# Performance work log

Measured on AMD Instinct MI355X. Metric: run time of the kernel, lower is better.

The kernel has to match this reference:

```python
import jax, jax.numpy as jnp
import numpy as np

LN_EPS = 1e-5  # torch LayerNorm default
EPSILON = 1e-8  # slot attention epsilon


def layer_norm(x, g, b):
    mu = jnp.mean(x, axis=-1, keepdims=True)
    var = jnp.var(x, axis=-1, keepdims=True)
    return (x - mu) * jax.lax.rsqrt(var + LN_EPS) * g + b


def setup_inputs() -> dict:
    key = jax.random.key(0)
    ks = jax.random.split(key, 12)
    B, N, S, D, M = 64, 4096, 8, 256, 1024
    s = 0.02
    return {
        "features": jax.random.normal(ks[0], (B, N, D), jnp.float32),
        "slots_init": jax.random.normal(ks[1], (B, S, D), jnp.float32),
        # LayerNorm params (feature, slots, mlp)
        "g_feat": jnp.ones((D,), jnp.float32), "b_feat": jnp.zeros((D,), jnp.float32),
        "g_slots": jnp.ones((D,), jnp.float32), "b_slots": jnp.zeros((D,), jnp.float32),
        "g_mlp": jnp.ones((D,), jnp.float32), "b_mlp": jnp.zeros((D,), jnp.float32),
        # k/v/q projections (torch Linear weight: [out,in], no bias)
        "Wk": jax.random.normal(ks[2], (D, D), jnp.float32) * s,
        "Wv": jax.random.normal(ks[3], (D, D), jnp.float32) * s,
        "Wq": jax.random.normal(ks[4], (D, D), jnp.float32) * s,
        # GRUCell params: weight_ih/hh [3D, D] (gate order r, z, n), biases [3D]
        "w_ih": jax.random.normal(ks[5], (3 * D, D), jnp.float32) * s,
        "w_hh": jax.random.normal(ks[6], (3 * D, D), jnp.float32) * s,
        "b_ih": jnp.zeros((3 * D,), jnp.float32),
        "b_hh": jnp.zeros((3 * D,), jnp.float32),
        # MLP: Linear(D->M), ReLU, Linear(M->D)
        "W1": jax.random.normal(ks[7], (M, D), jnp.float32) * s,
        "b1": jnp.zeros((M,), jnp.float32),
        "W2": jax.random.normal(ks[8], (D, M), jnp.float32) * s,
        "b2": jnp.zeros((D,), jnp.float32),
        "num_iter": 3,
    }


def gru_cell(x, h, w_ih, w_hh, b_ih, b_hh):
    # x, h: [B*, D]; torch.nn.GRUCell math, gate order r, z, n
    gi = x @ w_ih.T + b_ih  # [B*, 3D]
    gh = h @ w_hh.T + b_hh
    i_r, i_z, i_n = jnp.split(gi, 3, axis=-1)
    h_r, h_z, h_n = jnp.split(gh, 3, axis=-1)
    r = jax.nn.sigmoid(i_r + h_r)
    z = jax.nn.sigmoid(i_z + h_z)
    n = jnp.tanh(i_n + r * h_n)
    return (1.0 - z) * n + z * h


def reference(features, slots_init, g_feat, b_feat, g_slots, b_slots, g_mlp, b_mlp,
              Wk, Wv, Wq, w_ih, w_hh, b_ih, b_hh, W1, b1, W2, b2, num_iter):
    feats = layer_norm(features, g_feat, b_feat)          # [B, N, D]
    k = feats @ Wk.T                                      # [B, N, D]
    v = feats @ Wv.T                                      # [B, N, D]
    B, N, D = v.shape
    scale = D ** -0.5
    slots = slots_init                                    # [B, S, D]
    S = slots.shape[1]
    attn = None
    for _ in range(num_iter):
        slots_prev = slots
        q = layer_norm(slots, g_slots, b_slots) @ Wq.T    # [B, S, D]
        attn_logits = jnp.einsum('bid,bjd->bij', q, k) * scale  # [B, S, N]
        attn = jax.nn.softmax(attn_logits, axis=1)        # softmax over slots
        attn = attn + EPSILON
        attn_wm = attn / jnp.sum(attn, axis=-1, keepdims=True)
        updates = jnp.einsum('bij,bjd->bid', attn_wm, v)  # [B, S, D]
        slots = gru_cell(updates.reshape(-1, D), slots_prev.reshape(-1, D),
                         w_ih, w_hh, b_ih, b_hh).reshape(B, S, D)
        h = jax.nn.relu(layer_norm(slots, g_mlp, b_mlp) @ W1.T + b1)
        slots = slots + h @ W2.T + b2
    return slots, attn
```

## Files before the change

### kernel.cpp

```cpp
#include <hip/hip_runtime.h>
#include <stdint.h>

typedef unsigned short u16;
typedef unsigned int u32;
typedef __bf16 bf16_t;
typedef bf16_t bf16x8 __attribute__((ext_vector_type(8)));
typedef float f32x4 __attribute__((ext_vector_type(4)));

#define DEV static __device__ __forceinline__

DEV float bf2f(u16 a) {
  union { u32 u; float f; } c; c.u = ((u32)a) << 16; return c.f;
}
DEV u16 f2bf(float f) {
  union { float f; u32 u; } c; c.f = f;
  return (u16)((c.u + 0x7FFFu + ((c.u >> 16) & 1u)) >> 16);
}
DEV f32x4 mfma16(bf16x8 a, bf16x8 b, f32x4 c) {
  return __builtin_amdgcn_mfma_f32_16x16x32_bf16(a, b, c, 0, 0, 0);
}
DEV float wave_sum(float v) {
#pragma unroll
  for (int off = 32; off > 0; off >>= 1) v += __shfl_xor(v, off, 64);
  return v;
}
DEV float sum16(float v) {
  v += __shfl_xor(v, 1, 64);
  v += __shfl_xor(v, 2, 64);
  v += __shfl_xor(v, 4, 64);
  v += __shfl_xor(v, 8, 64);
  return v;
}

__global__ void __launch_bounds__(256) init_prep(
    const float* __restrict__ Wk, const float* __restrict__ Wv,
    const float* __restrict__ slots_init,
    const float* __restrict__ Wq, const float* __restrict__ w_ih,
    const float* __restrict__ w_hh, const float* __restrict__ W1,
    const float* __restrict__ W2,
    float* __restrict__ slots,
    u16* __restrict__ wqb, u16* __restrict__ wihb, u16* __restrict__ whhb,
    u16* __restrict__ w1b, u16* __restrict__ w2b,
    u16* __restrict__ wvb, u16* __restrict__ wktb) {
  const int blk = blockIdx.x;
  const int tid = threadIdx.x;
  if (blk < 128) {
    const int idx = blk * 1024 + tid * 4;
    *(float4*)(slots + idx) = *(const float4*)(slots_init + idx);
  } else if (blk < 1152) {
    const int i = (blk - 128) * 1024 + tid * 4;
    const float* src; u16* dst; int off;
    if (i < 65536)       { src = Wq;   dst = wqb;  off = i; }
    else if (i < 262144) { src = w_ih; dst = wihb; off = i - 65536; }
    else if (i < 458752) { src = w_hh; dst = whhb; off = i - 262144; }
    else if (i < 720896) { src = W1;   dst = w1b;  off = i - 458752; }
    else if (i < 983040) { src = W2;   dst = w2b;  off = i - 720896; }
    else                 { src = Wv;   dst = wvb;  off = i - 983040; }
    float4 v = *(const float4*)(src + off);
    *(ushort4*)(dst + off) = make_ushort4(f2bf(v.x), f2bf(v.y), f2bf(v.z), f2bf(v.w));
  } else {
    __shared__ u16 tl[64][66];
    const int tb = blk - 1152;
    const int r0 = (tb >> 2) * 64;
    const int c0 = (tb & 3) * 64;
    const int r = tid >> 2;
    const int cseg = (tid & 3) * 16;
#pragma unroll
    for (int q = 0; q < 4; q++) {
      float4 v = *(const float4*)(Wk + (size_t)(r0 + r) * 256 + c0 + cseg + q * 4);
      tl[r][cseg + q * 4 + 0] = f2bf(v.x);
      tl[r][cseg + q * 4 + 1] = f2bf(v.y);
      tl[r][cseg + q * 4 + 2] = f2bf(v.z);
      tl[r][cseg + q * 4 + 3] = f2bf(v.w);
    }
    __syncthreads();
    const int c = tid >> 2;
    const int rseg = (tid & 3) * 16;
    u16 out[16];
#pragma unroll
    for (int j = 0; j < 16; j++) out[j] = tl[rseg + j][c];
#pragma unroll
    for (int q = 0; q < 4; q++)
      *(ushort4*)(wktb + (size_t)(c0 + c) * 256 + r0 + rseg + q * 4) =
          make_ushort4(out[q * 4], out[q * 4 + 1], out[q * 4 + 2], out[q * 4 + 3]);
  }
}

__global__ void __launch_bounds__(256) ln_feat(
    const float* __restrict__ feat, const float* __restrict__ g,
    const float* __restrict__ bia,
    u16* __restrict__ fbuf, u16* __restrict__ fbuf_t) {
  __shared__ u16 T[64 * 264];
  const int tid = threadIdx.x;
  const int M0 = blockIdx.x * 64;
  const int b = M0 >> 12;
  const int nb = M0 & 4095;

#pragma unroll 2
  for (int i = 0; i < 8; i++) {
    const int gr = i * 256 + tid;
    const int m = gr >> 5;
    const int kc = gr & 31;
    const float* fp = feat + (size_t)(M0 + m) * 256 + kc * 8;
    float4 a0 = *(const float4*)fp;
    float4 a1 = *(const float4*)(fp + 4);
    float t1 = a0.x + a0.y + a0.z + a0.w + a1.x + a1.y + a1.z + a1.w;
    float t2 = a0.x * a0.x + a0.y * a0.y + a0.z * a0.z + a0.w * a0.w +
               a1.x * a1.x + a1.y * a1.y + a1.z * a1.z + a1.w * a1.w;
    t1 += __shfl_xor(t1, 1, 64);  t2 += __shfl_xor(t2, 1, 64);
    t1 += __shfl_xor(t1, 2, 64);  t2 += __shfl_xor(t2, 2, 64);
    t1 += __shfl_xor(t1, 4, 64);  t2 += __shfl_xor(t2, 4, 64);
    t1 += __shfl_xor(t1, 8, 64);  t2 += __shfl_xor(t2, 8, 64);
    t1 += __shfl_xor(t1, 16, 64); t2 += __shfl_xor(t2, 16, 64);
    const float mu = t1 * (1.f / 256.f);
    const float rs = rsqrtf(t2 * (1.f / 256.f) - mu * mu + 1e-5f);
    float4 g0 = *(const float4*)(g + kc * 8);
    float4 g1 = *(const float4*)(g + kc * 8 + 4);
    float4 b0 = *(const float4*)(bia + kc * 8);
    float4 b1 = *(const float4*)(bia + kc * 8 + 4);
    u16 y[8];
    y[0] = f2bf((a0.x - mu) * rs * g0.x + b0.x);
    y[1] = f2bf((a0.y - mu) * rs * g0.y + b0.y);
    y[2] = f2bf((a0.z - mu) * rs * g0.z + b0.z);
    y[3] = f2bf((a0.w - mu) * rs * g0.w + b0.w);
    y[4] = f2bf((a1.x - mu) * rs * g1.x + b1.x);
    y[5] = f2bf((a1.y - mu) * rs * g1.y + b1.y);
    y[6] = f2bf((a1.z - mu) * rs * g1.z + b1.z);
    y[7] = f2bf((a1.w - mu) * rs * g1.w + b1.w);
    uint4 pk = make_uint4((u32)y[0] | ((u32)y[1] << 16), (u32)y[2] | ((u32)y[3] << 16),
                          (u32)y[4] | ((u32)y[5] << 16), (u32)y[6] | ((u32)y[7] << 16));
    *(uint4*)&T[m * 264 + kc * 8] = pk;
    *(uint4*)(fbuf + (size_t)(M0 + m) * 256 + kc * 8) = pk;
  }
  __syncthreads();

  const int dl = tid >> 4;
  const int ns4 = (tid & 15) * 4;
#pragma unroll 4
  for (int o = 0; o < 16; o++) {
    const int d = dl + o * 16;
    u16 v0 = T[(ns4 + 0) * 264 + d];
    u16 v1 = T[(ns4 + 1) * 264 + d];
    u16 v2 = T[(ns4 + 2) * 264 + d];
    u16 v3 = T[(ns4 + 3) * 264 + d];
    *(ushort4*)(fbuf_t + ((size_t)b * 256 + d) * 4096 + nb + ns4) = make_ushort4(v0, v1, v2, v3);
  }
}

__global__ void __launch_bounds__(256) attn_pass(
    const float* __restrict__ slots, const float* __restrict__ gs, const float* __restrict__ bs,
    const u16* __restrict__ wqb, const u16* __restrict__ wktb,
    const u16* __restrict__ fbuf, const u16* __restrict__ fbuf_t,
    float* __restrict__ part_acc, float* __restrict__ part_den,
    float* __restrict__ attn_out, int store_attn) {
  __shared__ u16 pt[16 * 264];
  __shared__ u16 qld[16 * 264];
  const int chunk = blockIdx.x;
  const int b = blockIdx.y;
  const int n0 = chunk * 256;
  const int tid = threadIdx.x;
  const int lane = tid & 63;
  const int wv = tid >> 6;
  const int cl = lane & 15;
  const int rq = lane >> 4;
  const f32x4 Z = {0.f, 0.f, 0.f, 0.f};

  for (int i = tid; i < 8 * 264; i += 256) pt[8 * 264 + i] = 0;
  for (int rr = 0; rr < 2; rr++) {
    const int s = wv * 2 + rr;
    float4 x4 = *(const float4*)(slots + ((size_t)b * 8 + s) * 256 + lane * 4);
    float x[4] = {x4.x, x4.y, x4.z, x4.w};
    float s1 = x[0] + x[1] + x[2] + x[3];
    float s2 = x[0] * x[0] + x[1] * x[1] + x[2] * x[2] + x[3] * x[3];
    s1 = wave_sum(s1);
    s2 = wave_sum(s2);
    float mu = s1 * (1.f / 256.f);
    float rstd = rsqrtf(s2 * (1.f / 256.f) - mu * mu + 1e-5f);
    float4 g4 = *(const float4*)(gs + lane * 4);
    float4 b4 = *(const float4*)(bs + lane * 4);
    u16 o4[4];
    o4[0] = f2bf((x[0] - mu) * rstd * g4.x + b4.x);
    o4[1] = f2bf((x[1] - mu) * rstd * g4.y + b4.y);
    o4[2] = f2bf((x[2] - mu) * rstd * g4.z + b4.z);
    o4[3] = f2bf((x[3] - mu) * rstd * g4.w + b4.w);
    *(ushort4*)&pt[s * 264 + lane * 4] = make_ushort4(o4[0], o4[1], o4[2], o4[3]);
  }
  __syncthreads();

  {
    bf16x8 af[8];
#pragma unroll
    for (int ks = 0; ks < 8; ks++)
      af[ks] = *(const bf16x8*)&pt[cl * 264 + ks * 32 + rq * 8];
#pragma unroll
    for (int t = 0; t < 4; t++) {
      const int of = wv * 64 + t * 16;
      f32x4 acc = Z;
#pragma unroll
      for (int ks = 0; ks < 8; ks++) {
        bf16x8 bw = *(const bf16x8*)(wqb + (size_t)(of + cl) * 256 + ks * 32 + rq * 8);
        acc = mfma16(af[ks], bw, acc);
      }
#pragma unroll
      for (int r = 0; r < 4; r++)
        qld[(rq * 4 + r) * 264 + of + cl] = f2bf(acc[r]);
    }
  }
  __syncthreads();

  {
    bf16x8 a2[8];
#pragma unroll
    for (int ks = 0; ks < 8; ks++)
      a2[ks] = *(const bf16x8*)&qld[cl * 264 + ks * 32 + rq * 8];
#pragma unroll
    for (int t = 0; t < 4; t++) {
      const int of = wv * 64 + t * 16;
      f32x4 acc = Z;
#pragma unroll
      for (int ks = 0; ks < 8; ks++) {
        bf16x8 bw = *(const bf16x8*)(wktb + (size_t)(of + cl) * 256 + ks * 32 + rq * 8);
        acc = mfma16(a2[ks], bw, acc);
      }
#pragma unroll
      for (int r = 0; r < 4; r++)
        pt[(rq * 4 + r) * 264 + of + cl] = f2bf(acc[r]);
    }
  }
  __syncthreads();

  bf16x8 aq[8];
#pragma unroll
  for (int ks = 0; ks < 8; ks++)
    aq[ks] = *(const bf16x8*)&pt[cl * 264 + ks * 32 + rq * 8];

  float dacc[4] = {0.f, 0.f, 0.f, 0.f};
#pragma unroll
  for (int t = 0; t < 4; t++) {
    const int nl = (wv * 4 + t) * 16;
    f32x4 acc = Z;
    const int n = n0 + nl + cl;
#pragma unroll
    for (int ks = 0; ks < 8; ks++) {
      bf16x8 bk = *(const bf16x8*)(fbuf + ((size_t)b * 4096 + n) * 256 + ks * 32 + rq * 8);
      acc = mfma16(aq[ks], bk, acc);
    }
    float l[4];
#pragma unroll
    for (int r = 0; r < 4; r++) l[r] = acc[r] * 0.0625f;
    float m4 = fmaxf(fmaxf(l[0], l[1]), fmaxf(l[2], l[3]));
    float m8 = fmaxf(m4, __shfl_xor(m4, 16, 64));
    float e[4];
    float s4 = 0.f;
#pragma unroll
    for (int r = 0; r < 4; r++) { e[r] = __expf(l[r] - m8); s4 += e[r]; }
    float s8 = s4 + __shfl_xor(s4, 16, 64);
    float inv = 1.f / s8;
    float pa[4];
#pragma unroll
    for (int r = 0; r < 4; r++) pa[r] = e[r] * inv + 1e-8f;
#pragma unroll
    for (int r = 0; r < 4; r++) qld[(rq * 4 + r) * 264 + nl + cl] = f2bf(pa[r]);
    if (store_attn && lane < 32) {
#pragma unroll
      for (int r = 0; r < 4; r++)
        attn_out[((size_t)b * 8 + rq * 4 + r) * 4096 + n0 + nl + cl] = pa[r];
    }
#pragma unroll
    for (int r = 0; r < 4; r++) dacc[r] += sum16(pa[r]);
  }
  if (cl == 0 && lane < 32) {
#pragma unroll
    for (int r = 0; r < 4; r++)
      part_den[(((size_t)b * 16 + chunk) * 4 + wv) * 8 + rq * 4 + r] = dacc[r];
  }
  __syncthreads();

  bf16x8 ap[8];
#pragma unroll
  for (int ks = 0; ks < 8; ks++)
    ap[ks] = *(const bf16x8*)&qld[cl * 264 + ks * 32 + rq * 8];
#pragma unroll
  for (int t = 0; t < 4; t++) {
    const int df = wv * 64 + t * 16;
    f32x4 acc = Z;
    const int d = df + cl;
#pragma unroll
    for (int ks = 0; ks < 8; ks++) {
      bf16x8 bv = *(const bf16x8*)(fbuf_t + ((size_t)b * 256 + d) * 4096 + n0 + ks * 32 + rq * 8);
      acc = mfma16(ap[ks], bv, acc);
    }
    if (lane < 32) {
#pragma unroll
      for (int r = 0; r < 4; r++)
        part_acc[(((size_t)b * 16 + chunk) * 8 + rq * 4 + r) * 256 + d] = acc[r];
    }
  }
}

__global__ void __launch_bounds__(256) slot_update(
    const float* __restrict__ part_acc, const float* __restrict__ part_den,
    float* __restrict__ slots,
    const u16* __restrict__ wihb, const u16* __restrict__ whhb,
    const float* __restrict__ b_ih, const float* __restrict__ b_hh,
    const float* __restrict__ gm, const float* __restrict__ bm,
    const u16* __restrict__ w1b, const float* __restrict__ b1,
    const u16* __restrict__ w2b, const float* __restrict__ b2,
    const u16* __restrict__ wvb,
    float* __restrict__ slots_out, int last) {
  __shared__ u16 ubf[16 * 264];
  __shared__ u16 hbf[16 * 264];
  __shared__ u16 updbf[16 * 264];
  __shared__ float hf32[8 * 256];
  __shared__ float midf[8 * 256];
  __shared__ u16 h1bf[16 * 1032];
  __shared__ float denl[8];
  const int b = blockIdx.x;
  const int tid = threadIdx.x;
  const int lane = tid & 63;
  const int wv = tid >> 6;
  const int cl = lane & 15;
  const int rq = lane >> 4;
  const f32x4 Z = {0.f, 0.f, 0.f, 0.f};

  for (int i = tid; i < 8 * 264; i += 256) { ubf[8 * 264 + i] = 0; hbf[8 * 264 + i] = 0; }
  if (tid < 8) {
    float s = 0.f;
    for (int c = 0; c < 64; c++) s += part_den[((size_t)b * 64 + c) * 8 + tid];
    denl[tid] = s;
  }
  __syncthreads();

#pragma unroll
  for (int i = 0; i < 8; i++) {
    float s = 0.f;
#pragma unroll
    for (int c = 0; c < 16; c++)
      s += part_acc[(((size_t)b * 16 + c) * 8 + i) * 256 + tid];
    float u = s / denl[i];
    ubf[i * 264 + tid] = f2bf(u);
    float h = slots[((size_t)b * 8 + i) * 256 + tid];
    hf32[i * 256 + tid] = h;
    hbf[i * 264 + tid] = f2bf(h);
  }
  __syncthreads();

  {
    bf16x8 apf[8];
#pragma unroll
    for (int ks = 0; ks < 8; ks++)
      apf[ks] = *(const bf16x8*)&ubf[cl * 264 + ks * 32 + rq * 8];
#pragma unroll
    for (int t = 0; t < 4; t++) {
      const int of = wv * 64 + t * 16;
      f32x4 acc = Z;
#pragma unroll
      for (int ks = 0; ks < 8; ks++) {
        bf16x8 bw = *(const bf16x8*)(wvb + (size_t)(of + cl) * 256 + ks * 32 + rq * 8);
        acc = mfma16(apf[ks], bw, acc);
      }
#pragma unroll
      for (int r = 0; r < 4; r++)
        updbf[(rq * 4 + r) * 264 + of + cl] = f2bf(acc[r]);
    }
  }
  __syncthreads();

  bf16x8 au[8], ah[8];
#pragma unroll
  for (int ks = 0; ks < 8; ks++) {
    au[ks] = *(const bf16x8*)&updbf[cl * 264 + ks * 32 + rq * 8];
    ah[ks] = *(const bf16x8*)&hbf[cl * 264 + ks * 32 + rq * 8];
  }
#pragma unroll
  for (int j4 = 0; j4 < 4; j4++) {
    const int j = wv * 4 + j4;
    f32x4 a_ir = Z, a_iz = Z, a_in = Z, a_hr = Z, a_hz = Z, a_hn = Z;
#pragma unroll
    for (int ks = 0; ks < 8; ks++) {
      const int koff = ks * 32 + rq * 8;
      const int o_r = j * 16 + cl;
      bf16x8 bri = *(const bf16x8*)(wihb + (size_t)o_r * 256 + koff);
      bf16x8 bzi = *(const bf16x8*)(wihb + (size_t)(256 + o_r) * 256 + koff);
      bf16x8 bni = *(const bf16x8*)(wihb + (size_t)(512 + o_r) * 256 + koff);
      bf16x8 brh = *(const bf16x8*)(whhb + (size_t)o_r * 256 + koff);
      bf16x8 bzh = *(const bf16x8*)(whhb + (size_t)(256 + o_r) * 256 + koff);
      bf16x8 bnh = *(const bf16x8*)(whhb + (size_t)(512 + o_r) * 256 + koff);
      a_ir = mfma16(au[ks], bri, a_ir);
      a_iz = mfma16(au[ks], bzi, a_iz);
      a_in = mfma16(au[ks], bni, a_in);
      a_hr = mfma16(ah[ks], brh, a_hr);
      a_hz = mfma16(ah[ks], bzh, a_hz);
      a_hn = mfma16(ah[ks], bnh, a_hn);
    }
    if (lane < 32) {
      const int d = j * 16 + cl;
      const float bihr = b_ih[d], bihz = b_ih[256 + d], bihn = b_ih[512 + d];
      const float bhhr = b_hh[d], bhhz = b_hh[256 + d], bhhn = b_hh[512 + d];
#pragma unroll
      for (int r = 0; r < 4; r++) {
        const int s = rq * 4 + r;
        float ir = a_ir[r] + bihr, iz = a_iz[r] + bihz, inn = a_in[r] + bihn;
        float hr = a_hr[r] + bhhr, hz = a_hz[r] + bhhz, hn = a_hn[r] + bhhn;
        float rg = 1.f / (1.f + __expf(-(ir + hr)));
        float zg = 1.f / (1.f + __expf(-(iz + hz)));
        float ng = tanhf(inn + rg * hn);
        float h = hf32[s * 256 + d];
        midf[s * 256 + d] = (1.f - zg) * ng + zg * h;
      }
    }
  }
  __syncthreads();

  for (int rr = 0; rr < 2; rr++) {
    const int s = wv * 2 + rr;
    float4 x4 = *(const float4*)&midf[s * 256 + lane * 4];
    float x[4] = {x4.x, x4.y, x4.z, x4.w};
    float s1 = x[0] + x[1] + x[2] + x[3];
    float s2 = x[0] * x[0] + x[1] * x[1] + x[2] * x[2] + x[3] * x[3];
    s1 = wave_sum(s1);
    s2 = wave_sum(s2);
    float mu = s1 * (1.f / 256.f);
    float rstd = rsqrtf(s2 * (1.f / 256.f) - mu * mu + 1e-5f);
    float4 g4 = *(const float4*)(gm + lane * 4);
    float4 b4 = *(const float4*)(bm + lane * 4);
    u16 o4[4];
    o4[0] = f2bf((x[0] - mu) * rstd * g4.x + b4.x);
    o4[1] = f2bf((x[1] - mu) * rstd * g4.y + b4.y);
    o4[2] = f2bf((x[2] - mu) * rstd * g4.z + b4.z);
    o4[3] = f2bf((x[3] - mu) * rstd * g4.w + b4.w);
    *(ushort4*)&ubf[s * 264 + lane * 4] = make_ushort4(o4[0], o4[1], o4[2], o4[3]);
  }
  __syncthreads();

  bf16x8 al[8];
#pragma unroll
  for (int ks = 0; ks < 8; ks++)
    al[ks] = *(const bf16x8*)&ubf[cl * 264 + ks * 32 + rq * 8];
#pragma unroll
  for (int t = 0; t < 16; t++) {
    const int of = wv * 256 + t * 16;
    f32x4 acc = Z;
#pragma unroll
    for (int ks = 0; ks < 8; ks++) {
      bf16x8 bw = *(const bf16x8*)(w1b + (size_t)(of + cl) * 256 + ks * 32 + rq * 8);
      acc = mfma16(al[ks], bw, acc);
    }
    const float bb = b1[of + cl];
#pragma unroll
    for (int r = 0; r < 4; r++)
      h1bf[(rq * 4 + r) * 1032 + of + cl] = f2bf(fmaxf(acc[r] + bb, 0.f));
  }
  __syncthreads();

  f32x4 acc2[4] = {Z, Z, Z, Z};
  for (int ks = 0; ks < 32; ks++) {
    bf16x8 ah1 = *(const bf16x8*)&h1bf[cl * 1032 + ks * 32 + rq * 8];
#pragma unroll
    for (int t = 0; t < 4; t++) {
      const int o = wv * 64 + t * 16 + cl;
      bf16x8 bw = *(const bf16x8*)(w2b + (size_t)o * 1024 + ks * 32 + rq * 8);
      acc2[t] = mfma16(ah1, bw, acc2[t]);
    }
  }
  if (lane < 32) {
#pragma unroll
    for (int t = 0; t < 4; t++) {
      const int o = wv * 64 + t * 16 + cl;
      const float bb = b2[o];
#pragma unroll
      for (int r = 0; r < 4; r++) {
        const int s = rq * 4 + r;
        float val = midf[s * 256 + o] + acc2[t][r] + bb;
        slots[((size_t)b * 8 + s) * 256 + o] = val;
        if (last) slots_out[((size_t)b * 8 + s) * 256 + o] = val;
      }
    }
  }
}

extern "C" void kernel_launch(void* const* d_in, const int* in_sizes, int n_in,
                              void* d_out, int out_size, void* d_ws, size_t ws_size,
                              hipStream_t stream) {
  (void)in_sizes; (void)n_in; (void)out_size;
  const float* features = (const float*)d_in[0];
  const float* slots_init = (const float*)d_in[1];
  const float* g_feat = (const float*)d_in[2];
  const float* b_feat = (const float*)d_in[3];
  const float* g_slots = (const float*)d_in[4];
  const float* b_slots = (const float*)d_in[5];
  const float* g_mlp = (const float*)d_in[6];
  const float* b_mlp = (const float*)d_in[7];
  const float* Wk = (const float*)d_in[8];
  const float* Wv = (const float*)d_in[9];
  const float* Wq = (const float*)d_in[10];
  const float* w_ih = (const float*)d_in[11];
  const float* w_hh = (const float*)d_in[12];
  const float* b_ih = (const float*)d_in[13];
  const float* b_hh = (const float*)d_in[14];
  const float* W1 = (const float*)d_in[15];
  const float* b1 = (const float*)d_in[16];
  const float* W2 = (const float*)d_in[17];
  const float* b2 = (const float*)d_in[18];

  const size_t REQUIRED = 280236032ull;
  if (ws_size < REQUIRED) return;

  char* ws = (char*)d_ws;
  u16* fbuf = (u16*)(ws + 0);
  u16* fbuf_t = (u16*)(ws + 134217728);
  float* part_acc = (float*)(ws + 268959744);
  float* part_den = (float*)(ws + 277348352);
  float* slots = (float*)(ws + 277479424);
  u16* wktb = (u16*)(ws + 278003712);
  u16* wvb = (u16*)(ws + 278134784);
  u16* wqb = (u16*)(ws + 278269952);
  u16* wihb = (u16*)(ws + 278401024);
  u16* whhb = (u16*)(ws + 278794240);
  u16* w1b = (u16*)(ws + 279187456);
  u16* w2b = (u16*)(ws + 279711744);

  float* out_slots = (float*)d_out;
  float* out_attn = out_slots + 131072;

  init_prep<<<1168, 256, 0, stream>>>(Wk, Wv, slots_init, Wq, w_ih, w_hh, W1, W2,
                                      slots, wqb, wihb, whhb, w1b, w2b, wvb, wktb);
  ln_feat<<<4096, 256, 0, stream>>>(features, g_feat, b_feat, fbuf, fbuf_t);
  for (int it = 0; it < 3; it++) {
    attn_pass<<<dim3(16, 64), 256, 0, stream>>>(slots, g_slots, b_slots, wqb, wktb,
                                                fbuf, fbuf_t, part_acc, part_den,
                                                out_attn, it == 2 ? 1 : 0);
    slot_update<<<64, 256, 0, stream>>>(part_acc, part_den, slots, wihb, whhb, b_ih, b_hh,
                                        g_mlp, b_mlp, w1b, b1, w2b, b2, wvb,
                                        out_slots, it == 2 ? 1 : 0);
  }
}
```

Before: 891.4 us.

## Drop transposed feature buffer; stage feature tiles in swizzled LDS for both GEMMs

```diff
diff --git a/kernel.cpp b/kernel.cpp
--- a/kernel.cpp
+++ b/kernel.cpp
@@ -88,14 +88,9 @@
 
 __global__ void __launch_bounds__(256) ln_feat(
     const float* __restrict__ feat, const float* __restrict__ g,
-    const float* __restrict__ bia,
-    u16* __restrict__ fbuf, u16* __restrict__ fbuf_t) {
-  __shared__ u16 T[64 * 264];
+    const float* __restrict__ bia, u16* __restrict__ fbuf) {
   const int tid = threadIdx.x;
   const int M0 = blockIdx.x * 64;
-  const int b = M0 >> 12;
-  const int nb = M0 & 4095;
-
 #pragma unroll 2
   for (int i = 0; i < 8; i++) {
     const int gr = i * 256 + tid;
@@ -129,35 +124,17 @@
     y[7] = f2bf((a1.w - mu) * rs * g1.w + b1.w);
     uint4 pk = make_uint4((u32)y[0] | ((u32)y[1] << 16), (u32)y[2] | ((u32)y[3] << 16),
                           (u32)y[4] | ((u32)y[5] << 16), (u32)y[6] | ((u32)y[7] << 16));
-    *(uint4*)&T[m * 264 + kc * 8] = pk;
     *(uint4*)(fbuf + (size_t)(M0 + m) * 256 + kc * 8) = pk;
   }
-  __syncthreads();
-
-  const int dl = tid >> 4;
-  const int ns4 = (tid & 15) * 4;
-#pragma unroll 4
-  for (int o = 0; o < 16; o++) {
-    const int d = dl + o * 16;
-    u16 v0 = T[(ns4 + 0) * 264 + d];
-    u16 v1 = T[(ns4 + 1) * 264 + d];
-    u16 v2 = T[(ns4 + 2) * 264 + d];
-    u16 v3 = T[(ns4 + 3) * 264 + d];
-    *(ushort4*)(fbuf_t + ((size_t)b * 256 + d) * 4096 + nb + ns4) = make_ushort4(v0, v1, v2, v3);
-  }
-}
-
-__global__ void __launch_bounds__(256) attn_pass(
+}
+
+__global__ void __launch_bounds__(256) slot_qk(
     const float* __restrict__ slots, const float* __restrict__ gs, const float* __restrict__ bs,
     const u16* __restrict__ wqb, const u16* __restrict__ wktb,
-    const u16* __restrict__ fbuf, const u16* __restrict__ fbuf_t,
-    float* __restrict__ part_acc, float* __restrict__ part_den,
-    float* __restrict__ attn_out, int store_attn) {
-  __shared__ u16 pt[16 * 264];
+    u16* __restrict__ qkbuf) {
+  __shared__ u16 lnb[16 * 264];
   __shared__ u16 qld[16 * 264];
-  const int chunk = blockIdx.x;
-  const int b = blockIdx.y;
-  const int n0 = chunk * 256;
+  const int b = blockIdx.x;
   const int tid = threadIdx.x;
   const int lane = tid & 63;
   const int wv = tid >> 6;
@@ -165,7 +142,8 @@
   const int rq = lane >> 4;
   const f32x4 Z = {0.f, 0.f, 0.f, 0.f};
 
-  for (int i = tid; i < 8 * 264; i += 256) pt[8 * 264 + i] = 0;
+  for (int i = tid; i < 8 * 264; i += 256) lnb[8 * 264 + i] = 0;
+
   for (int rr = 0; rr < 2; rr++) {
     const int s = wv * 2 + rr;
     float4 x4 = *(const float4*)(slots + ((size_t)b * 8 + s) * 256 + lane * 4);
@@ -183,7 +161,7 @@
     o4[1] = f2bf((x[1] - mu) * rstd * g4.y + b4.y);
     o4[2] = f2bf((x[2] - mu) * rstd * g4.z + b4.z);
     o4[3] = f2bf((x[3] - mu) * rstd * g4.w + b4.w);
-    *(ushort4*)&pt[s * 264 + lane * 4] = make_ushort4(o4[0], o4[1], o4[2], o4[3]);
+    *(ushort4*)&lnb[s * 264 + lane * 4] = make_ushort4(o4[0], o4[1], o4[2], o4[3]);
   }
   __syncthreads();
 
@@ -191,7 +169,7 @@
     bf16x8 af[8];
 #pragma unroll
     for (int ks = 0; ks < 8; ks++)
-      af[ks] = *(const bf16x8*)&pt[cl * 264 + ks * 32 + rq * 8];
+      af[ks] = *(const bf16x8*)&lnb[cl * 264 + ks * 32 + rq * 8];
 #pragma unroll
     for (int t = 0; t < 4; t++) {
       const int of = wv * 64 + t * 16;
@@ -224,25 +202,53 @@
       }
 #pragma unroll
       for (int r = 0; r < 4; r++)
-        pt[(rq * 4 + r) * 264 + of + cl] = f2bf(acc[r]);
-    }
-  }
-  __syncthreads();
+        qkbuf[(size_t)b * 4096 + (rq * 4 + r) * 256 + of + cl] = f2bf(acc[r]);
+    }
+  }
+}
+
+__global__ void __launch_bounds__(256) attn_pass(
+    const u16* __restrict__ qkbuf, const u16* __restrict__ fbuf,
+    float* __restrict__ part_acc, float* __restrict__ part_den,
+    float* __restrict__ attn_out, int store_attn) {
+  __shared__ u16 Asm[64 * 264];
+  __shared__ u16 pt[16 * 72];
+  const int chunk = blockIdx.x;
+  const int b = blockIdx.y;
+  const int n0 = chunk * 64;
+  const int tid = threadIdx.x;
+  const int lane = tid & 63;
+  const int wv = tid >> 6;
+  const int cl = lane & 15;
+  const int rq = lane >> 4;
+  const f32x4 Z = {0.f, 0.f, 0.f, 0.f};
+
+  const u16* fsrc = fbuf + ((size_t)b * 4096 + n0) * 256;
+#pragma unroll
+  for (int i = 0; i < 8; i++) {
+    const int gr = i * 256 + tid;
+    const int m = gr >> 5;
+    const int kc = gr & 31;
+    uint4 v = *(const uint4*)(fsrc + (size_t)m * 256 + kc * 8);
+    const int sw = (kc & 24) | ((kc & 7) ^ (m & 7) ^ ((m >> 3) & 7));
+    *(uint4*)&Asm[m * 264 + sw * 8] = v;
+  }
 
   bf16x8 aq[8];
 #pragma unroll
   for (int ks = 0; ks < 8; ks++)
-    aq[ks] = *(const bf16x8*)&pt[cl * 264 + ks * 32 + rq * 8];
-
-  float dacc[4] = {0.f, 0.f, 0.f, 0.f};
-#pragma unroll
-  for (int t = 0; t < 4; t++) {
-    const int nl = (wv * 4 + t) * 16;
+    aq[ks] = *(const bf16x8*)(qkbuf + (size_t)b * 4096 + cl * 256 + ks * 32 + rq * 8);
+  __syncthreads();
+
+  {
+    const int nl = wv * 16;
+    const int n = nl + cl;
     f32x4 acc = Z;
-    const int n = n0 + nl + cl;
 #pragma unroll
     for (int ks = 0; ks < 8; ks++) {
-      bf16x8 bk = *(const bf16x8*)(fbuf + ((size_t)b * 4096 + n) * 256 + ks * 32 + rq * 8);
+      const int c = ks * 4 + rq;
+      const int ca = (c & 24) | ((c & 7) ^ (n & 7) ^ ((n >> 3) & 7));
+      bf16x8 bk = *(const bf16x8*)&Asm[n * 264 + ca * 8];
       acc = mfma16(aq[ks], bk, acc);
     }
     float l[4];
@@ -260,40 +266,46 @@
 #pragma unroll
     for (int r = 0; r < 4; r++) pa[r] = e[r] * inv + 1e-8f;
 #pragma unroll
-    for (int r = 0; r < 4; r++) qld[(rq * 4 + r) * 264 + nl + cl] = f2bf(pa[r]);
+    for (int r = 0; r < 4; r++) pt[(rq * 4 + r) * 72 + nl + cl] = f2bf(pa[r]);
     if (store_attn && lane < 32) {
 #pragma unroll
       for (int r = 0; r < 4; r++)
         attn_out[((size_t)b * 8 + rq * 4 + r) * 4096 + n0 + nl + cl] = pa[r];
     }
-#pragma unroll
-    for (int r = 0; r < 4; r++) dacc[r] += sum16(pa[r]);
-  }
-  if (cl == 0 && lane < 32) {
-#pragma unroll
-    for (int r = 0; r < 4; r++)
-      part_den[(((size_t)b * 16 + chunk) * 4 + wv) * 8 + rq * 4 + r] = dacc[r];
-  }
-  __syncthreads();
-
-  bf16x8 ap[8];
-#pragma unroll
-  for (int ks = 0; ks < 8; ks++)
-    ap[ks] = *(const bf16x8*)&qld[cl * 264 + ks * 32 + rq * 8];
+    float dacc[4];
+#pragma unroll
+    for (int r = 0; r < 4; r++) dacc[r] = sum16(pa[r]);
+    if (cl == 0 && lane < 32) {
+#pragma unroll
+      for (int r = 0; r < 4; r++)
+        part_den[(((size_t)b * 64 + chunk) * 4 + wv) * 8 + rq * 4 + r] = dacc[r];
+    }
+  }
+  __syncthreads();
+
 #pragma unroll
   for (int t = 0; t < 4; t++) {
-    const int df = wv * 64 + t * 16;
+    const int d = wv * 64 + t * 16 + cl;
+    const int dchunk = d >> 3;
+    const int doff = d & 7;
     f32x4 acc = Z;
-    const int d = df + cl;
-#pragma unroll
-    for (int ks = 0; ks < 8; ks++) {
-      bf16x8 bv = *(const bf16x8*)(fbuf_t + ((size_t)b * 256 + d) * 4096 + n0 + ks * 32 + rq * 8);
-      acc = mfma16(ap[ks], bv, acc);
+#pragma unroll
+    for (int ks = 0; ks < 2; ks++) {
+      const int r0 = ks * 32 + rq * 8;
+      const int cx = (ks * 4 + rq) & 7;
+      union { u16 w[8]; bf16x8 v; } bv;
+#pragma unroll
+      for (int j = 0; j < 8; j++) {
+        const int ca = (dchunk & 24) | ((dchunk & 7) ^ j ^ cx);
+        bv.w[j] = Asm[(r0 + j) * 264 + ca * 8 + doff];
+      }
+      bf16x8 pa8 = *(const bf16x8*)&pt[cl * 72 + r0];
+      acc = mfma16(pa8, bv.v, acc);
     }
     if (lane < 32) {
 #pragma unroll
       for (int r = 0; r < 4; r++)
-        part_acc[(((size_t)b * 16 + chunk) * 8 + rq * 4 + r) * 256 + d] = acc[r];
+        part_acc[(((size_t)b * 64 + chunk) * 8 + rq * 4 + r) * 256 + d] = acc[r];
     }
   }
 }
@@ -314,6 +326,7 @@
   __shared__ float hf32[8 * 256];
   __shared__ float midf[8 * 256];
   __shared__ u16 h1bf[16 * 1032];
+  __shared__ float denp[64];
   __shared__ float denl[8];
   const int b = blockIdx.x;
   const int tid = threadIdx.x;
@@ -324,19 +337,27 @@
   const f32x4 Z = {0.f, 0.f, 0.f, 0.f};
 
   for (int i = tid; i < 8 * 264; i += 256) { ubf[8 * 264 + i] = 0; hbf[8 * 264 + i] = 0; }
+  if (tid < 64) {
+    const int s = tid & 7, g = tid >> 3;
+    float sum = 0.f;
+    for (int e = g * 32; e < g * 32 + 32; e++)
+      sum += part_den[((size_t)b * 256 + e) * 8 + s];
+    denp[tid] = sum;
+  }
+  __syncthreads();
   if (tid < 8) {
-    float s = 0.f;
-    for (int c = 0; c < 64; c++) s += part_den[((size_t)b * 64 + c) * 8 + tid];
-    denl[tid] = s;
+    float s2 = 0.f;
+    for (int g = 0; g < 8; g++) s2 += denp[g * 8 + tid];
+    denl[tid] = s2;
   }
   __syncthreads();
 
 #pragma unroll
   for (int i = 0; i < 8; i++) {
     float s = 0.f;
-#pragma unroll
-    for (int c = 0; c < 16; c++)
-      s += part_acc[(((size_t)b * 16 + c) * 8 + i) * 256 + tid];
+#pragma unroll 8
+    for (int c = 0; c < 64; c++)
+      s += part_acc[(((size_t)b * 64 + c) * 8 + i) * 256 + tid];
     float u = s / denl[i];
     ubf[i * 264 + tid] = f2bf(u);
     float h = slots[((size_t)b * 8 + i) * 256 + tid];
@@ -503,32 +524,32 @@
   const float* W2 = (const float*)d_in[17];
   const float* b2 = (const float*)d_in[18];
 
-  const size_t REQUIRED = 280236032ull;
+  const size_t REQUIRED = 171573248ull;
   if (ws_size < REQUIRED) return;
 
   char* ws = (char*)d_ws;
   u16* fbuf = (u16*)(ws + 0);
-  u16* fbuf_t = (u16*)(ws + 134217728);
-  float* part_acc = (float*)(ws + 268959744);
-  float* part_den = (float*)(ws + 277348352);
-  float* slots = (float*)(ws + 277479424);
-  u16* wktb = (u16*)(ws + 278003712);
-  u16* wvb = (u16*)(ws + 278134784);
-  u16* wqb = (u16*)(ws + 278269952);
-  u16* wihb = (u16*)(ws + 278401024);
-  u16* whhb = (u16*)(ws + 278794240);
-  u16* w1b = (u16*)(ws + 279187456);
-  u16* w2b = (u16*)(ws + 279711744);
+  float* part_acc = (float*)(ws + 134217728);
+  float* part_den = (float*)(ws + 167772160);
+  u16* qkbuf = (u16*)(ws + 168296448);
+  float* slots = (float*)(ws + 168820736);
+  u16* wktb = (u16*)(ws + 169345024);
+  u16* wvb = (u16*)(ws + 169476096);
+  u16* wqb = (u16*)(ws + 169607168);
+  u16* wihb = (u16*)(ws + 169738240);
+  u16* whhb = (u16*)(ws + 170131456);
+  u16* w1b = (u16*)(ws + 170524672);
+  u16* w2b = (u16*)(ws + 171048960);
 
   float* out_slots = (float*)d_out;
   float* out_attn = out_slots + 131072;
 
   init_prep<<<1168, 256, 0, stream>>>(Wk, Wv, slots_init, Wq, w_ih, w_hh, W1, W2,
                                       slots, wqb, wihb, whhb, w1b, w2b, wvb, wktb);
-  ln_feat<<<4096, 256, 0, stream>>>(features, g_feat, b_feat, fbuf, fbuf_t);
+  ln_feat<<<4096, 256, 0, stream>>>(features, g_feat, b_feat, fbuf);
   for (int it = 0; it < 3; it++) {
-    attn_pass<<<dim3(16, 64), 256, 0, stream>>>(slots, g_slots, b_slots, wqb, wktb,
-                                                fbuf, fbuf_t, part_acc, part_den,
+    slot_qk<<<64, 256, 0, stream>>>(slots, g_slots, b_slots, wqb, wktb, qkbuf);
+    attn_pass<<<dim3(64, 64), 256, 0, stream>>>(qkbuf, fbuf, part_acc, part_den,
                                                 out_attn, it == 2 ? 1 : 0);
     slot_update<<<64, 256, 0, stream>>>(part_acc, part_den, slots, wihb, whhb, b_ih, b_hh,
                                         g_mlp, b_mlp, w1b, b1, w2b, b2, wvb,
```

After: 837.5 us. 1.06x faster.

## Split slot query projection into separate kernel and restructure attention value GEMM

Applied to the files above, without the earlier changes.

```diff
diff --git a/kernel.cpp b/kernel.cpp
--- a/kernel.cpp
+++ b/kernel.cpp
@@ -147,17 +147,13 @@
   }
 }
 
-__global__ void __launch_bounds__(256) attn_pass(
+__global__ void __launch_bounds__(256) slot_qk(
     const float* __restrict__ slots, const float* __restrict__ gs, const float* __restrict__ bs,
     const u16* __restrict__ wqb, const u16* __restrict__ wktb,
-    const u16* __restrict__ fbuf, const u16* __restrict__ fbuf_t,
-    float* __restrict__ part_acc, float* __restrict__ part_den,
-    float* __restrict__ attn_out, int store_attn) {
-  __shared__ u16 pt[16 * 264];
+    u16* __restrict__ qkbuf) {
+  __shared__ u16 lnb[16 * 264];
   __shared__ u16 qld[16 * 264];
-  const int chunk = blockIdx.x;
-  const int b = blockIdx.y;
-  const int n0 = chunk * 256;
+  const int b = blockIdx.x;
   const int tid = threadIdx.x;
   const int lane = tid & 63;
   const int wv = tid >> 6;
@@ -165,7 +161,8 @@
   const int rq = lane >> 4;
   const f32x4 Z = {0.f, 0.f, 0.f, 0.f};
 
-  for (int i = tid; i < 8 * 264; i += 256) pt[8 * 264 + i] = 0;
+  for (int i = tid; i < 8 * 264; i += 256) lnb[8 * 264 + i] = 0;
+
   for (int rr = 0; rr < 2; rr++) {
     const int s = wv * 2 + rr;
     float4 x4 = *(const float4*)(slots + ((size_t)b * 8 + s) * 256 + lane * 4);
@@ -183,7 +180,7 @@
     o4[1] = f2bf((x[1] - mu) * rstd * g4.y + b4.y);
     o4[2] = f2bf((x[2] - mu) * rstd * g4.z + b4.z);
     o4[3] = f2bf((x[3] - mu) * rstd * g4.w + b4.w);
-    *(ushort4*)&pt[s * 264 + lane * 4] = make_ushort4(o4[0], o4[1], o4[2], o4[3]);
+    *(ushort4*)&lnb[s * 264 + lane * 4] = make_ushort4(o4[0], o4[1], o4[2], o4[3]);
   }
   __syncthreads();
 
@@ -191,7 +188,7 @@
     bf16x8 af[8];
 #pragma unroll
     for (int ks = 0; ks < 8; ks++)
-      af[ks] = *(const bf16x8*)&pt[cl * 264 + ks * 32 + rq * 8];
+      af[ks] = *(const bf16x8*)&lnb[cl * 264 + ks * 32 + rq * 8];
 #pragma unroll
     for (int t = 0; t < 4; t++) {
       const int of = wv * 64 + t * 16;
@@ -224,22 +221,39 @@
       }
 #pragma unroll
       for (int r = 0; r < 4; r++)
-        pt[(rq * 4 + r) * 264 + of + cl] = f2bf(acc[r]);
-    }
-  }
-  __syncthreads();
+        qkbuf[(size_t)b * 4096 + (rq * 4 + r) * 256 + of + cl] = f2bf(acc[r]);
+    }
+  }
+}
+
+__global__ void __launch_bounds__(256, 4) attn_pass(
+    const u16* __restrict__ qkbuf, const u16* __restrict__ fbuf,
+    const u16* __restrict__ fbuf_t,
+    float* __restrict__ part_acc, float* __restrict__ part_den,
+    float* __restrict__ attn_out, int store_attn) {
+  __shared__ u16 pt[8 * 264];
+  __shared__ float outp[8 * 260];
+  const int sub = blockIdx.x;
+  const int b = blockIdx.y;
+  const int n0 = sub * 256;
+  const int tid = threadIdx.x;
+  const int lane = tid & 63;
+  const int wv = tid >> 6;
+  const int cl = lane & 15;
+  const int rq = lane >> 4;
+  const f32x4 Z = {0.f, 0.f, 0.f, 0.f};
 
   bf16x8 aq[8];
 #pragma unroll
   for (int ks = 0; ks < 8; ks++)
-    aq[ks] = *(const bf16x8*)&pt[cl * 264 + ks * 32 + rq * 8];
+    aq[ks] = *(const bf16x8*)(qkbuf + (size_t)b * 4096 + cl * 256 + ks * 32 + rq * 8);
 
   float dacc[4] = {0.f, 0.f, 0.f, 0.f};
 #pragma unroll
   for (int t = 0; t < 4; t++) {
-    const int nl = (wv * 4 + t) * 16;
+    const int nl = wv * 64 + t * 16;
+    const int n = n0 + nl + cl;
     f32x4 acc = Z;
-    const int n = n0 + nl + cl;
 #pragma unroll
     for (int ks = 0; ks < 8; ks++) {
       bf16x8 bk = *(const bf16x8*)(fbuf + ((size_t)b * 4096 + n) * 256 + ks * 32 + rq * 8);
@@ -259,8 +273,10 @@
     float pa[4];
 #pragma unroll
     for (int r = 0; r < 4; r++) pa[r] = e[r] * inv + 1e-8f;
-#pragma unroll
-    for (int r = 0; r < 4; r++) qld[(rq * 4 + r) * 264 + nl + cl] = f2bf(pa[r]);
+    if (lane < 32) {
+#pragma unroll
+      for (int r = 0; r < 4; r++) pt[(rq * 4 + r) * 264 + nl + cl] = f2bf(pa[r]);
+    }
     if (store_attn && lane < 32) {
 #pragma unroll
       for (int r = 0; r < 4; r++)
@@ -272,30 +288,34 @@
   if (cl == 0 && lane < 32) {
 #pragma unroll
     for (int r = 0; r < 4; r++)
-      part_den[(((size_t)b * 16 + chunk) * 4 + wv) * 8 + rq * 4 + r] = dacc[r];
-  }
-  __syncthreads();
-
-  bf16x8 ap[8];
-#pragma unroll
-  for (int ks = 0; ks < 8; ks++)
-    ap[ks] = *(const bf16x8*)&qld[cl * 264 + ks * 32 + rq * 8];
-#pragma unroll
-  for (int t = 0; t < 4; t++) {
-    const int df = wv * 64 + t * 16;
-    f32x4 acc = Z;
-    const int d = df + cl;
-#pragma unroll
-    for (int ks = 0; ks < 8; ks++) {
-      bf16x8 bv = *(const bf16x8*)(fbuf_t + ((size_t)b * 256 + d) * 4096 + n0 + ks * 32 + rq * 8);
-      acc = mfma16(ap[ks], bv, acc);
-    }
-    if (lane < 32) {
+      part_den[(((size_t)b * 16 + sub) * 4 + wv) * 8 + rq * 4 + r] = dacc[r];
+  }
+  __syncthreads();
+
+  f32x4 acc2[4] = {Z, Z, Z, Z};
+#pragma unroll
+  for (int ks = 0; ks < 8; ks++) {
+    const int noff = ks * 32 + rq * 8;
+    bf16x8 bp = *(const bf16x8*)&pt[(cl & 7) * 264 + noff];
+#pragma unroll
+    for (int dt = 0; dt < 4; dt++) {
+      const int d = wv * 64 + dt * 16 + cl;
+      bf16x8 af = *(const bf16x8*)(fbuf_t + ((size_t)b * 256 + d) * 4096 + n0 + noff);
+      acc2[dt] = mfma16(af, bp, acc2[dt]);
+    }
+  }
+  if (cl < 8) {
+#pragma unroll
+    for (int dt = 0; dt < 4; dt++)
 #pragma unroll
       for (int r = 0; r < 4; r++)
-        part_acc[(((size_t)b * 16 + chunk) * 8 + rq * 4 + r) * 256 + d] = acc[r];
-    }
-  }
+        outp[cl * 260 + wv * 64 + dt * 16 + rq * 4 + r] = acc2[dt][r];
+  }
+  __syncthreads();
+
+#pragma unroll
+  for (int i = 0; i < 8; i++)
+    part_acc[(((size_t)b * 16 + sub) * 8 + i) * 256 + tid] = outp[i * 260 + tid];
 }
 
 __global__ void __launch_bounds__(256) slot_update(
@@ -509,6 +529,7 @@
   char* ws = (char*)d_ws;
   u16* fbuf = (u16*)(ws + 0);
   u16* fbuf_t = (u16*)(ws + 134217728);
+  u16* qkbuf = (u16*)(ws + 268435456);
   float* part_acc = (float*)(ws + 268959744);
   float* part_den = (float*)(ws + 277348352);
   float* slots = (float*)(ws + 277479424);
@@ -527,8 +548,8 @@
                                       slots, wqb, wihb, whhb, w1b, w2b, wvb, wktb);
   ln_feat<<<4096, 256, 0, stream>>>(features, g_feat, b_feat, fbuf, fbuf_t);
   for (int it = 0; it < 3; it++) {
-    attn_pass<<<dim3(16, 64), 256, 0, stream>>>(slots, g_slots, b_slots, wqb, wktb,
-                                                fbuf, fbuf_t, part_acc, part_den,
+    slot_qk<<<64, 256, 0, stream>>>(slots, g_slots, b_slots, wqb, wktb, qkbuf);
+    attn_pass<<<dim3(16, 64), 256, 0, stream>>>(qkbuf, fbuf, fbuf_t, part_acc, part_den,
                                                 out_attn, it == 2 ? 1 : 0);
     slot_update<<<64, 256, 0, stream>>>(part_acc, part_den, slots, wihb, whhb, b_ih, b_hh,
                                         g_mlp, b_mlp, w1b, b1, w2b, b2, wvb,
```

Result: faster. 830.2 us (-6.9%).
